# Performance work log

Hardware: AMD Instinct MI355X
Metric: run time of the kernel (lower is better)

The kernel has to match this reference:

```python
import jax, jax.numpy as jnp
import numpy as np

N = 200000
D = 256
B = 512  # fixed num_segments (batch.max()+1 in the torch code)
LN_EPS = 1e-5


def _layernorm(h, gamma, beta):
    mu = jnp.mean(h, axis=-1, keepdims=True)
    var = jnp.var(h, axis=-1, keepdims=True)
    return (h - mu) * jax.lax.rsqrt(var + LN_EPS) * gamma + beta


def setup_inputs() -> dict:
    key = jax.random.key(0)
    ks = jax.random.split(key, 10)
    x = jax.random.normal(ks[0], (N, D), dtype=jnp.float32)
    batch = jnp.sort(jax.random.randint(ks[1], (N,), 0, B)).astype(jnp.int64)
    s = 0.05
    return {
        "x": x,
        "batch": batch,
        "vn_embed": jax.random.normal(ks[2], (1, D), dtype=jnp.float32) * 0.02,
        "W1": jax.random.normal(ks[3], (D, D), dtype=jnp.float32) * s,
        "b1": jnp.zeros((D,), dtype=jnp.float32),
        "g1": jnp.ones((D,), dtype=jnp.float32),
        "be1": jnp.zeros((D,), dtype=jnp.float32),
        "W2": jax.random.normal(ks[4], (D, D), dtype=jnp.float32) * s,
        "b2": jnp.zeros((D,), dtype=jnp.float32),
        "g2": jnp.ones((D,), dtype=jnp.float32),
        "be2": jnp.zeros((D,), dtype=jnp.float32),
        "Wg": jax.random.normal(ks[5], (2 * D, D), dtype=jnp.float32) * s,
        "bg": jnp.zeros((D,), dtype=jnp.float32),
    }


def reference(x, batch, vn_embed, W1, b1, g1, be1, W2, b2, g2, be2, Wg, bg):
    # scatter-mean: per-graph average of node features  [B, D]
    seg_sum = jax.ops.segment_sum(x, batch, num_segments=B)
    cnt = jax.ops.segment_sum(jnp.ones((x.shape[0],), x.dtype), batch, num_segments=B)
    node_agg = seg_sum / jnp.maximum(cnt, 1.0)[:, None]
    # node_to_vn: Linear + GELU(exact) + LayerNorm (dropout = identity at eval)
    vn_update = _layernorm(jax.nn.gelu(node_agg @ W1 + b1, approximate=False), g1, be1)
    vn_state = vn_embed + vn_update  # vn_embed broadcasts [1,D] -> [B,D]
    # gather broadcast back to nodes + vn_to_node MLP
    vn_broadcast = vn_state[batch]  # [N, D]
    node_update = _layernorm(jax.nn.gelu(vn_broadcast @ W2 + b2, approximate=False), g2, be2)
    # sigmoid gate on concat + gated residual
    gate = jax.nn.sigmoid(jnp.concatenate([x, node_update], axis=-1) @ Wg + bg)
    x_out = x + gate * node_update
    return (x_out, vn_state)
```

## Files before the change

kernel.cpp:

```cpp
#include <hip/hip_runtime.h>
#include <hip/hip_bf16.h>
#include <math.h>

#define DIM 256
#define B_SEG 512
#define LN_EPS 1e-5f

typedef __attribute__((ext_vector_type(8))) short bf16x8;
typedef __attribute__((ext_vector_type(4))) float f32x4;

__device__ __forceinline__ float gelu_exact(float v) {
    return 0.5f * v * (1.0f + erff(v * 0.70710678118654752f));
}

__device__ __forceinline__ unsigned int pack2bf(float a, float b) {
    unsigned int ua = (unsigned int)__bfloat16_as_ushort(__float2bfloat16(a));
    unsigned int ub = (unsigned int)__bfloat16_as_ushort(__float2bfloat16(b));
    return ua | (ub << 16);
}

__device__ __forceinline__ void async16(const void* g, void* l) {
    __builtin_amdgcn_global_load_lds(
        (const __attribute__((address_space(1))) void*)(g),
        (__attribute__((address_space(3))) void*)(l), 16, 0, 0);
}

__global__ __launch_bounds__(256) void k_prep(const float* __restrict__ Wg,
                                              __hip_bfloat16* __restrict__ Wt2,
                                              const int* __restrict__ batch,
                                              int* __restrict__ seg_start, int n) {
    if (blockIdx.x < 256) {
        int k = blockIdx.x;
        int c = threadIdx.x;
        Wt2[((size_t)(k >> 3) << 11) + (c << 3) + (k & 7)] = __float2bfloat16(Wg[(size_t)k * DIM + c]);
        return;
    }
    for (int s = threadIdx.x; s <= B_SEG; s += 256) {
        int lo = 0, hi = n;
        while (lo < hi) {
            int mid = (lo + hi) >> 1;
            if (batch[mid] < s) lo = mid + 1; else hi = mid;
        }
        seg_start[s] = lo;
    }
}

__global__ __launch_bounds__(256) void k_pass1(const float* __restrict__ x,
                                               const int* __restrict__ batch,
                                               float* __restrict__ part,
                                               unsigned int* __restrict__ hdr,
                                               float* __restrict__ extra,
                                               __hip_bfloat16* __restrict__ xbf,
                                               int n, int emit) {
    const int tile = blockIdx.x;
    const int i0   = tile * 64;
    if (i0 >= n) return;
    const int iN   = min(i0 + 64, n);

    const int wave = threadIdx.x >> 6;
    const int lane = threadIdx.x & 63;
    const int d4   = lane * 4;
    const int dby  = lane * 8;

    const int sf = batch[i0];
    const int sl = batch[iN - 1];

    float4 accA = make_float4(0.f, 0.f, 0.f, 0.f);
    float4 accB = make_float4(0.f, 0.f, 0.f, 0.f);

    #pragma unroll
    for (int g = 0; g < 4; ++g) {
        int   bt[4];
        float4 v[4];
        #pragma unroll
        for (int jj = 0; jj < 4; ++jj) {
            int r = i0 + g * 16 + 4 * jj + wave;
            bt[jj] = (r < iN) ? batch[r] : -2;
        }
        #pragma unroll
        for (int jj = 0; jj < 4; ++jj) {
            int r = i0 + g * 16 + 4 * jj + wave;
            v[jj] = (r < iN) ? *(const float4*)(x + (size_t)r * DIM + d4)
                             : make_float4(0.f, 0.f, 0.f, 0.f);
        }
        __builtin_amdgcn_sched_barrier(0);
        #pragma unroll
        for (int jj = 0; jj < 4; ++jj) {
            int r = i0 + g * 16 + 4 * jj + wave;
            if (emit && r < iN) {
                uint2 pk;
                pk.x = pack2bf(v[jj].x, v[jj].y);
                pk.y = pack2bf(v[jj].z, v[jj].w);
                *(uint2*)((char*)xbf + (size_t)r * 512 + (dby ^ ((r & 7) << 4))) = pk;
            }
            if (bt[jj] == sf) {
                accA.x += v[jj].x; accA.y += v[jj].y; accA.z += v[jj].z; accA.w += v[jj].w;
            } else if (bt[jj] == sl) {
                accB.x += v[jj].x; accB.y += v[jj].y; accB.z += v[jj].z; accB.w += v[jj].w;
            } else if (r < iN) {
                atomicAdd(&extra[(size_t)bt[jj] * DIM + d4 + 0], v[jj].x);
                atomicAdd(&extra[(size_t)bt[jj] * DIM + d4 + 1], v[jj].y);
                atomicAdd(&extra[(size_t)bt[jj] * DIM + d4 + 2], v[jj].z);
                atomicAdd(&extra[(size_t)bt[jj] * DIM + d4 + 3], v[jj].w);
            }
        }
    }

    __shared__ float4 redA[4][64];
    __shared__ float4 redB[4][64];
    redA[wave][lane] = accA;
    redB[wave][lane] = accB;
    __syncthreads();
    if (wave == 0) {
        float4 a0 = redA[0][lane], a1 = redA[1][lane], a2 = redA[2][lane], a3 = redA[3][lane];
        float4 t;
        t.x = (a0.x + a1.x) + (a2.x + a3.x);
        t.y = (a0.y + a1.y) + (a2.y + a3.y);
        t.z = (a0.z + a1.z) + (a2.z + a3.z);
        t.w = (a0.w + a1.w) + (a2.w + a3.w);
        *(float4*)(part + ((size_t)tile * 2 + 0) * DIM + d4) = t;
        if (lane == 0) hdr[tile] = (unsigned int)sf | ((unsigned int)sl << 16);
    } else if (wave == 1) {
        float4 a0 = redB[0][lane], a1 = redB[1][lane], a2 = redB[2][lane], a3 = redB[3][lane];
        float4 t;
        t.x = (a0.x + a1.x) + (a2.x + a3.x);
        t.y = (a0.y + a1.y) + (a2.y + a3.y);
        t.z = (a0.z + a1.z) + (a2.z + a3.z);
        t.w = (a0.w + a1.w) + (a2.w + a3.w);
        *(float4*)(part + ((size_t)tile * 2 + 1) * DIM + d4) = t;
    }
}

__global__ __launch_bounds__(256) void k_vn(const float* __restrict__ part,
                                            const unsigned int* __restrict__ hdr,
                                            const float* __restrict__ extra,
                                            const int* __restrict__ seg_start,
                                            const float* __restrict__ vn_embed,
                                            const float* __restrict__ W1, const float* __restrict__ b1,
                                            const float* __restrict__ g1, const float* __restrict__ be1,
                                            const float* __restrict__ W2, const float* __restrict__ b2,
                                            const float* __restrict__ g2, const float* __restrict__ be2,
                                            const float* __restrict__ Wg, const float* __restrict__ bg,
                                            float* __restrict__ vn_state_out,
                                            float* __restrict__ nu,
                                            float* __restrict__ gpart,
                                            int use_parts) {
    __shared__ float sIn[DIM];
    __shared__ float sRed[DIM];
    __shared__ float sRed2[DIM];
    const int b = blockIdx.x;
    const int d = threadIdx.x;

    const int s0 = seg_start[b], s1 = seg_start[b + 1];
    float sum = extra[(size_t)b * DIM + d];
    if (use_parts && s1 > s0) {
        int t0 = s0 >> 6, t1 = (s1 - 1) >> 6;
        for (int t = t0; t <= t1; ++t) {
            unsigned int h = hdr[t];
            int f = (int)(h & 0xffffu), l = (int)(h >> 16);
            if (f == b) sum += part[((size_t)t * 2 + 0) * DIM + d];
            if (l == b && l != f) sum += part[((size_t)t * 2 + 1) * DIM + d];
        }
    }
    float denom = fmaxf((float)(s1 - s0), 1.0f);
    sIn[d] = sum / denom;
    __syncthreads();

    float h0 = 0.f, h1 = 0.f, h2a = 0.f, h3 = 0.f;
    for (int k = 0; k < DIM; k += 4) {
        h0  = fmaf(sIn[k + 0], W1[(size_t)(k + 0) * DIM + d], h0);
        h1  = fmaf(sIn[k + 1], W1[(size_t)(k + 1) * DIM + d], h1);
        h2a = fmaf(sIn[k + 2], W1[(size_t)(k + 2) * DIM + d], h2a);
        h3  = fmaf(sIn[k + 3], W1[(size_t)(k + 3) * DIM + d], h3);
    }
    float h = gelu_exact(b1[d] + ((h0 + h1) + (h2a + h3)));

    sRed[d] = h; sRed2[d] = h * h;
    __syncthreads();
    for (int s = 128; s > 0; s >>= 1) {
        if (d < s) { sRed[d] += sRed[d + s]; sRed2[d] += sRed2[d + s]; }
        __syncthreads();
    }
    float mu = sRed[0] * (1.0f / DIM);
    float var = fmaxf(sRed2[0] * (1.0f / DIM) - mu * mu, 0.0f);
    float rs = rsqrtf(var + LN_EPS);
    float vnst = vn_embed[d] + ((h - mu) * rs * g1[d] + be1[d]);
    vn_state_out[(size_t)b * DIM + d] = vnst;
    __syncthreads();
    sIn[d] = vnst;
    __syncthreads();

    float g0 = 0.f, g1a = 0.f, g2a = 0.f, g3 = 0.f;
    for (int k = 0; k < DIM; k += 4) {
        g0  = fmaf(sIn[k + 0], W2[(size_t)(k + 0) * DIM + d], g0);
        g1a = fmaf(sIn[k + 1], W2[(size_t)(k + 1) * DIM + d], g1a);
        g2a = fmaf(sIn[k + 2], W2[(size_t)(k + 2) * DIM + d], g2a);
        g3  = fmaf(sIn[k + 3], W2[(size_t)(k + 3) * DIM + d], g3);
    }
    float h2 = gelu_exact(b2[d] + ((g0 + g1a) + (g2a + g3)));

    sRed[d] = h2; sRed2[d] = h2 * h2;
    __syncthreads();
    for (int s = 128; s > 0; s >>= 1) {
        if (d < s) { sRed[d] += sRed[d + s]; sRed2[d] += sRed2[d + s]; }
        __syncthreads();
    }
    float mu2 = sRed[0] * (1.0f / DIM);
    float var2 = fmaxf(sRed2[0] * (1.0f / DIM) - mu2 * mu2, 0.0f);
    float rs2 = rsqrtf(var2 + LN_EPS);
    float nud = (h2 - mu2) * rs2 * g2[d] + be2[d];
    nu[(size_t)b * DIM + d] = nud;
    __syncthreads();
    sIn[d] = nud;
    __syncthreads();

    float p0 = 0.f, p1 = 0.f, p2 = 0.f, p3 = 0.f;
    for (int k = 0; k < DIM; k += 4) {
        p0 = fmaf(sIn[k + 0], Wg[(size_t)(DIM + k + 0) * DIM + d], p0);
        p1 = fmaf(sIn[k + 1], Wg[(size_t)(DIM + k + 1) * DIM + d], p1);
        p2 = fmaf(sIn[k + 2], Wg[(size_t)(DIM + k + 2) * DIM + d], p2);
        p3 = fmaf(sIn[k + 3], Wg[(size_t)(DIM + k + 3) * DIM + d], p3);
    }
    gpart[(size_t)b * DIM + d] = bg[d] + ((p0 + p1) + (p2 + p3));
}

__global__ __launch_bounds__(256, 4) void k_gate_bf(const __hip_bfloat16* __restrict__ xbf,
                                                    const int* __restrict__ batch,
                                                    const __hip_bfloat16* __restrict__ Wt2,
                                                    const float* __restrict__ nu,
                                                    const float* __restrict__ gpart,
                                                    float* __restrict__ xout,
                                                    int n) {
    __shared__ __align__(16) char sA[64 * 512];

    const int tid  = threadIdx.x;
    const int wave = tid >> 6;
    const int lane = tid & 63;
    const int r15  = lane & 15;
    const int kq   = lane >> 4;
    const size_t i0 = (size_t)blockIdx.x * 64;

    const char* gsrc = (const char*)xbf + i0 * 512;
    #pragma unroll
    for (int j = 0; j < 8; ++j)
        async16(gsrc + j * 4096 + tid * 16, sA + j * 4096 + wave * 1024);
    __syncthreads();

    f32x4 acc[4][4];
    #pragma unroll
    for (int m = 0; m < 4; ++m)
        #pragma unroll
        for (int nn = 0; nn < 4; ++nn)
            acc[m][nn] = (f32x4){0.f, 0.f, 0.f, 0.f};

    #pragma unroll
    for (int ks = 0; ks < 8; ++ks) {
        bf16x8 a[4], b[4];
        #pragma unroll
        for (int nn = 0; nn < 4; ++nn) {
            int c = wave * 64 + nn * 16 + r15;
            b[nn] = *(const bf16x8*)(Wt2 + ((size_t)(ks * 4 + kq) << 11) + (c << 3));
        }
        #pragma unroll
        for (int m = 0; m < 4; ++m) {
            int r = m * 16 + r15;
            a[m] = *(const bf16x8*)(sA + r * 512 + ((ks * 64 + kq * 16) ^ ((r & 7) << 4)));
        }
        #pragma unroll
        for (int m = 0; m < 4; ++m)
            #pragma unroll
            for (int nn = 0; nn < 4; ++nn)
                acc[m][nn] = __builtin_amdgcn_mfma_f32_16x16x32_bf16(a[m], b[nn], acc[m][nn], 0, 0, 0);
    }

    #pragma unroll
    for (int m = 0; m < 4; ++m) {
        #pragma unroll
        for (int q = 0; q < 4; ++q) {
            int rr = m * 16 + kq * 4 + q;
            long node = (long)(i0 + rr);
            if (node >= n) continue;
            int bb = batch[node];
            #pragma unroll
            for (int nn = 0; nn < 4; ++nn) {
                int col = wave * 64 + nn * 16 + r15;
                float pre = acc[m][nn][q] + gpart[bb * DIM + col];
                float e = __expf(-pre);
                float gte = __builtin_amdgcn_rcpf(1.0f + e);
                float xres = __bfloat162float(
                    *(const __hip_bfloat16*)(sA + rr * 512 + ((2 * col) ^ ((rr & 7) << 4))));
                xout[(size_t)node * DIM + col] = xres + gte * nu[bb * DIM + col];
            }
        }
    }
}

__global__ __launch_bounds__(256) void k_segsum_fp(const float* __restrict__ x,
                                                   const int* __restrict__ batch,
                                                   float* __restrict__ sums,
                                                   int n) {
    const int i0 = blockIdx.x * 64;
    if (i0 >= n) return;
    const int t    = threadIdx.x;
    const int lane = t & 63;
    const int d4   = lane * 4;
    const int rg   = t >> 6;
    float4 acc = make_float4(0.f, 0.f, 0.f, 0.f);
    int cur = -1;
    for (int j = 0; j < 16; ++j) {
        int i = i0 + rg + 4 * j;
        if (i >= n) break;
        int b = batch[i];
        if (b != cur) {
            if (cur >= 0) {
                atomicAdd(&sums[(size_t)cur * DIM + d4 + 0], acc.x);
                atomicAdd(&sums[(size_t)cur * DIM + d4 + 1], acc.y);
                atomicAdd(&sums[(size_t)cur * DIM + d4 + 2], acc.z);
                atomicAdd(&sums[(size_t)cur * DIM + d4 + 3], acc.w);
            }
            acc = make_float4(0.f, 0.f, 0.f, 0.f);
            cur = b;
        }
        float4 v = *(const float4*)(x + (size_t)i * DIM + d4);
        acc.x += v.x; acc.y += v.y; acc.z += v.z; acc.w += v.w;
    }
    if (cur >= 0) {
        atomicAdd(&sums[(size_t)cur * DIM + d4 + 0], acc.x);
        atomicAdd(&sums[(size_t)cur * DIM + d4 + 1], acc.y);
        atomicAdd(&sums[(size_t)cur * DIM + d4 + 2], acc.z);
        atomicAdd(&sums[(size_t)cur * DIM + d4 + 3], acc.w);
    }
}

__global__ __launch_bounds__(256) void k_gate_fp(const float* __restrict__ x,
                                                 const int* __restrict__ batch,
                                                 const __hip_bfloat16* __restrict__ Wt2,
                                                 const float* __restrict__ nu,
                                                 const float* __restrict__ gpart,
                                                 float* __restrict__ xout,
                                                 int n) {
    __shared__ __align__(16) char sA[32 * 512];
    const int tid  = threadIdx.x;
    const int wave = tid >> 6;
    const int lane = tid & 63;
    const int r15  = lane & 15;
    const int kq   = lane >> 4;
    const int i0   = blockIdx.x * 32;

    float4 av0[4], av1[4];
    #pragma unroll
    for (int j = 0; j < 4; ++j) {
        int v = j * 256 + tid;
        int r = v >> 5;
        int k8 = v & 31;
        int node = i0 + r;
        if (node < n) {
            const float* p = x + (size_t)node * DIM + k8 * 8;
            av0[j] = *(const float4*)p;
            av1[j] = *(const float4*)(p + 4);
        } else {
            av0[j] = make_float4(0.f, 0.f, 0.f, 0.f);
            av1[j] = av0[j];
        }
    }
    #pragma unroll
    for (int j = 0; j < 4; ++j) {
        int v = j * 256 + tid;
        int r = v >> 5;
        int k8 = v & 31;
        uint4 pk;
        pk.x = pack2bf(av0[j].x, av0[j].y);
        pk.y = pack2bf(av0[j].z, av0[j].w);
        pk.z = pack2bf(av1[j].x, av1[j].y);
        pk.w = pack2bf(av1[j].z, av1[j].w);
        *(uint4*)(sA + r * 512 + ((k8 * 16) ^ ((r & 7) << 4))) = pk;
    }
    __syncthreads();

    f32x4 acc[2][4];
    #pragma unroll
    for (int m = 0; m < 2; ++m)
        #pragma unroll
        for (int nn = 0; nn < 4; ++nn)
            acc[m][nn] = (f32x4){0.f, 0.f, 0.f, 0.f};

    #pragma unroll
    for (int ks = 0; ks < 8; ++ks) {
        bf16x8 a[2], b[4];
        #pragma unroll
        for (int nn = 0; nn < 4; ++nn) {
            int c = wave * 64 + nn * 16 + r15;
            b[nn] = *(const bf16x8*)(Wt2 + ((size_t)(ks * 4 + kq) << 11) + (c << 3));
        }
        #pragma unroll
        for (int m = 0; m < 2; ++m) {
            int r = m * 16 + r15;
            a[m] = *(const bf16x8*)(sA + r * 512 + ((ks * 64 + kq * 16) ^ ((r & 7) << 4)));
        }
        #pragma unroll
        for (int m = 0; m < 2; ++m)
            #pragma unroll
            for (int nn = 0; nn < 4; ++nn)
                acc[m][nn] = __builtin_amdgcn_mfma_f32_16x16x32_bf16(a[m], b[nn], acc[m][nn], 0, 0, 0);
    }

    #pragma unroll
    for (int m = 0; m < 2; ++m) {
        #pragma unroll
        for (int q = 0; q < 4; ++q) {
            int rr = m * 16 + kq * 4 + q;
            int node = i0 + rr;
            if (node >= n) continue;
            int bb = batch[node];
            #pragma unroll
            for (int nn = 0; nn < 4; ++nn) {
                int col = wave * 64 + nn * 16 + r15;
                float pre = acc[m][nn][q] + gpart[bb * DIM + col];
                float e = __expf(-pre);
                float gte = __builtin_amdgcn_rcpf(1.0f + e);
                float xres = __bfloat162float(
                    *(const __hip_bfloat16*)(sA + rr * 512 + ((2 * col) ^ ((rr & 7) << 4))));
                xout[(size_t)node * DIM + col] = xres + gte * nu[bb * DIM + col];
            }
        }
    }
}

extern "C" void kernel_launch(void* const* d_in, const int* in_sizes, int n_in,
                              void* d_out, int out_size, void* d_ws, size_t ws_size,
                              hipStream_t stream) {
    const float* x        = (const float*)d_in[0];
    const int*   batch    = (const int*)d_in[1];
    const float* vn_embed = (const float*)d_in[2];
    const float* W1  = (const float*)d_in[3];
    const float* b1  = (const float*)d_in[4];
    const float* g1  = (const float*)d_in[5];
    const float* be1 = (const float*)d_in[6];
    const float* W2  = (const float*)d_in[7];
    const float* b2  = (const float*)d_in[8];
    const float* g2  = (const float*)d_in[9];
    const float* be2 = (const float*)d_in[10];
    const float* Wg  = (const float*)d_in[11];
    const float* bg  = (const float*)d_in[12];

    const int n = in_sizes[0] / DIM;
    const int nt64 = (n + 63) / 64;

    float* out = (float*)d_out;
    float* xout = out;
    float* vn_state_out = out + (size_t)n * DIM;

    char* wsb = (char*)d_ws;
    int*          seg_start = (int*)wsb;
    unsigned int* hdr       = (unsigned int*)(wsb + 4096);
    float*        extra     = (float*)(wsb + 20480);
    float*        part      = (float*)(wsb + 544768);
    char*         after     = wsb + 544768 + (size_t)nt64 * 2 * DIM * 4;
    float* nu    = (float*)after;
    float* gpart = nu + (size_t)B_SEG * DIM;
    __hip_bfloat16* Wt2 = (__hip_bfloat16*)(gpart + (size_t)B_SEG * DIM);
    __hip_bfloat16* xbf = Wt2 + (size_t)DIM * DIM;

    const size_t xbf_off = (size_t)((char*)xbf - wsb);
    const size_t need = xbf_off + (size_t)nt64 * 64 * 512;
    const bool use_bf = (ws_size >= need);

    hipMemsetAsync(extra, 0, (size_t)B_SEG * DIM * sizeof(float), stream);

    k_prep<<<257, 256, 0, stream>>>(Wg, Wt2, batch, seg_start, n);

    if (use_bf) {
        k_pass1<<<nt64, 256, 0, stream>>>(x, batch, part, hdr, extra, xbf, n, 1);
    } else {
        k_segsum_fp<<<nt64, 256, 0, stream>>>(x, batch, extra, n);
    }

    k_vn<<<B_SEG, 256, 0, stream>>>(part, hdr, extra, seg_start, vn_embed,
                                    W1, b1, g1, be1,
                                    W2, b2, g2, be2,
                                    Wg, bg,
                                    vn_state_out, nu, gpart,
                                    use_bf ? 1 : 0);

    if (use_bf) {
        k_gate_bf<<<nt64, 256, 0, stream>>>(xbf, batch, Wt2, nu, gpart, xout, n);
    } else {
        int nblk3 = (n + 31) / 32;
        k_gate_fp<<<nblk3, 256, 0, stream>>>(x, batch, Wt2, nu, gpart, xout, n);
    }
}
```

Measured before the change: 200.3 us.

## Stage pass1 x tile into LDS via async global_load_lds and fold memset into prep

The segment-sum pass now copies the whole 64-row x tile into 64KB of shared memory with asynchronous global-to-LDS loads, then each wave walks 16 contiguous rows from LDS. The reduction buffers reuse the same shared memory. The separate memset of the atomic accumulator is removed and its zeroing is done by 128 extra blocks of the prep kernel, saving one launch. The 64KB LDS footprint per block limits occupancy to about two blocks per CU, which may reduce latency hiding compared with the previous register-based loads.

```diff
diff --git a/kernel.cpp b/kernel.cpp
--- a/kernel.cpp
+++ b/kernel.cpp
@@ -28,39 +28,61 @@
 __global__ __launch_bounds__(256) void k_prep(const float* __restrict__ Wg,
                                               __hip_bfloat16* __restrict__ Wt2,
                                               const int* __restrict__ batch,
-                                              int* __restrict__ seg_start, int n) {
+                                              int* __restrict__ seg_start,
+                                              float* __restrict__ extra, int n) {
     if (blockIdx.x < 256) {
         int k = blockIdx.x;
         int c = threadIdx.x;
         Wt2[((size_t)(k >> 3) << 11) + (c << 3) + (k & 7)] = __float2bfloat16(Wg[(size_t)k * DIM + c]);
         return;
     }
-    for (int s = threadIdx.x; s <= B_SEG; s += 256) {
-        int lo = 0, hi = n;
-        while (lo < hi) {
-            int mid = (lo + hi) >> 1;
-            if (batch[mid] < s) lo = mid + 1; else hi = mid;
-        }
-        seg_start[s] = lo;
-    }
-}
-
-__global__ __launch_bounds__(256) void k_pass1(const float* __restrict__ x,
-                                               const int* __restrict__ batch,
-                                               float* __restrict__ part,
-                                               unsigned int* __restrict__ hdr,
-                                               float* __restrict__ extra,
-                                               __hip_bfloat16* __restrict__ xbf,
-                                               int n, int emit) {
+    if (blockIdx.x == 256) {
+        for (int s = threadIdx.x; s <= B_SEG; s += 256) {
+            int lo = 0, hi = n;
+            while (lo < hi) {
+                int mid = (lo + hi) >> 1;
+                if (batch[mid] < s) lo = mid + 1; else hi = mid;
+            }
+            seg_start[s] = lo;
+        }
+        return;
+    }
+    int b = blockIdx.x - 257;
+    ((float4*)extra)[(size_t)b * 256 + threadIdx.x] = make_float4(0.f, 0.f, 0.f, 0.f);
+}
+
+__global__ __launch_bounds__(256, 2) void k_pass1(const float* __restrict__ x,
+                                                  const int* __restrict__ batch,
+                                                  float* __restrict__ part,
+                                                  unsigned int* __restrict__ hdr,
+                                                  float* __restrict__ extra,
+                                                  __hip_bfloat16* __restrict__ xbf,
+                                                  int n, int emit) {
+    __shared__ __align__(16) char sX[64 * 1024];
+
     const int tile = blockIdx.x;
     const int i0   = tile * 64;
     if (i0 >= n) return;
     const int iN   = min(i0 + 64, n);
 
-    const int wave = threadIdx.x >> 6;
-    const int lane = threadIdx.x & 63;
-    const int d4   = lane * 4;
-    const int dby  = lane * 8;
+    const int tid  = threadIdx.x;
+    const int wave = tid >> 6;
+    const int lane = tid & 63;
+
+    if (iN - i0 == 64) {
+        const char* gsrc = (const char*)x + (size_t)i0 * 1024;
+        #pragma unroll
+        for (int j = 0; j < 16; ++j)
+            async16(gsrc + j * 4096 + tid * 16, sX + j * 4096 + wave * 1024);
+    } else {
+        for (int v = tid; v < 64 * 64; v += 256) {
+            int r = v >> 6, c = v & 63;
+            float4 val = (i0 + r < n) ? *(const float4*)(x + (size_t)(i0 + r) * DIM + c * 4)
+                                      : make_float4(0.f, 0.f, 0.f, 0.f);
+            *(float4*)(sX + r * 1024 + c * 16) = val;
+        }
+    }
+    __syncthreads();
 
     const int sf = batch[i0];
     const int sl = batch[iN - 1];
@@ -68,66 +90,56 @@
     float4 accA = make_float4(0.f, 0.f, 0.f, 0.f);
     float4 accB = make_float4(0.f, 0.f, 0.f, 0.f);
 
-    #pragma unroll
-    for (int g = 0; g < 4; ++g) {
-        int   bt[4];
-        float4 v[4];
-        #pragma unroll
-        for (int jj = 0; jj < 4; ++jj) {
-            int r = i0 + g * 16 + 4 * jj + wave;
-            bt[jj] = (r < iN) ? batch[r] : -2;
-        }
-        #pragma unroll
-        for (int jj = 0; jj < 4; ++jj) {
-            int r = i0 + g * 16 + 4 * jj + wave;
-            v[jj] = (r < iN) ? *(const float4*)(x + (size_t)r * DIM + d4)
-                             : make_float4(0.f, 0.f, 0.f, 0.f);
-        }
-        __builtin_amdgcn_sched_barrier(0);
-        #pragma unroll
-        for (int jj = 0; jj < 4; ++jj) {
-            int r = i0 + g * 16 + 4 * jj + wave;
-            if (emit && r < iN) {
-                uint2 pk;
-                pk.x = pack2bf(v[jj].x, v[jj].y);
-                pk.y = pack2bf(v[jj].z, v[jj].w);
-                *(uint2*)((char*)xbf + (size_t)r * 512 + (dby ^ ((r & 7) << 4))) = pk;
-            }
-            if (bt[jj] == sf) {
-                accA.x += v[jj].x; accA.y += v[jj].y; accA.z += v[jj].z; accA.w += v[jj].w;
-            } else if (bt[jj] == sl) {
-                accB.x += v[jj].x; accB.y += v[jj].y; accB.z += v[jj].z; accB.w += v[jj].w;
-            } else if (r < iN) {
-                atomicAdd(&extra[(size_t)bt[jj] * DIM + d4 + 0], v[jj].x);
-                atomicAdd(&extra[(size_t)bt[jj] * DIM + d4 + 1], v[jj].y);
-                atomicAdd(&extra[(size_t)bt[jj] * DIM + d4 + 2], v[jj].z);
-                atomicAdd(&extra[(size_t)bt[jj] * DIM + d4 + 3], v[jj].w);
-            }
-        }
-    }
-
-    __shared__ float4 redA[4][64];
-    __shared__ float4 redB[4][64];
-    redA[wave][lane] = accA;
-    redB[wave][lane] = accB;
+    const int rbase = wave * 16;
+    #pragma unroll
+    for (int jj = 0; jj < 16; ++jj) {
+        const int r  = rbase + jj;
+        const int gr = i0 + r;
+        const bool valid = gr < n;
+        float4 v = *(const float4*)(sX + r * 1024 + lane * 16);
+        int b = valid ? batch[gr] : -2;
+        if (emit && valid) {
+            uint2 pk;
+            pk.x = pack2bf(v.x, v.y);
+            pk.y = pack2bf(v.z, v.w);
+            *(uint2*)((char*)xbf + (size_t)gr * 512 + ((lane * 8) ^ ((r & 7) << 4))) = pk;
+        }
+        if (b == sf) {
+            accA.x += v.x; accA.y += v.y; accA.z += v.z; accA.w += v.w;
+        } else if (b == sl) {
+            accB.x += v.x; accB.y += v.y; accB.z += v.z; accB.w += v.w;
+        } else if (valid) {
+            atomicAdd(&extra[(size_t)b * DIM + lane * 4 + 0], v.x);
+            atomicAdd(&extra[(size_t)b * DIM + lane * 4 + 1], v.y);
+            atomicAdd(&extra[(size_t)b * DIM + lane * 4 + 2], v.z);
+            atomicAdd(&extra[(size_t)b * DIM + lane * 4 + 3], v.w);
+        }
+    }
+
+    __syncthreads();
+    float4* red = (float4*)sX;
+    red[(wave * 2 + 0) * 64 + lane] = accA;
+    red[(wave * 2 + 1) * 64 + lane] = accB;
     __syncthreads();
     if (wave == 0) {
-        float4 a0 = redA[0][lane], a1 = redA[1][lane], a2 = redA[2][lane], a3 = redA[3][lane];
+        float4 a0 = red[0 * 64 + lane], a1 = red[2 * 64 + lane],
+               a2 = red[4 * 64 + lane], a3 = red[6 * 64 + lane];
         float4 t;
         t.x = (a0.x + a1.x) + (a2.x + a3.x);
         t.y = (a0.y + a1.y) + (a2.y + a3.y);
         t.z = (a0.z + a1.z) + (a2.z + a3.z);
         t.w = (a0.w + a1.w) + (a2.w + a3.w);
-        *(float4*)(part + ((size_t)tile * 2 + 0) * DIM + d4) = t;
+        *(float4*)(part + ((size_t)tile * 2 + 0) * DIM + lane * 4) = t;
         if (lane == 0) hdr[tile] = (unsigned int)sf | ((unsigned int)sl << 16);
     } else if (wave == 1) {
-        float4 a0 = redB[0][lane], a1 = redB[1][lane], a2 = redB[2][lane], a3 = redB[3][lane];
+        float4 a0 = red[1 * 64 + lane], a1 = red[3 * 64 + lane],
+               a2 = red[5 * 64 + lane], a3 = red[7 * 64 + lane];
         float4 t;
         t.x = (a0.x + a1.x) + (a2.x + a3.x);
         t.y = (a0.y + a1.y) + (a2.y + a3.y);
         t.z = (a0.z + a1.z) + (a2.z + a3.z);
         t.w = (a0.w + a1.w) + (a2.w + a3.w);
-        *(float4*)(part + ((size_t)tile * 2 + 1) * DIM + d4) = t;
+        *(float4*)(part + ((size_t)tile * 2 + 1) * DIM + lane * 4) = t;
     }
 }
 
@@ -465,9 +477,7 @@
     const size_t need = xbf_off + (size_t)nt64 * 64 * 512;
     const bool use_bf = (ws_size >= need);
 
-    hipMemsetAsync(extra, 0, (size_t)B_SEG * DIM * sizeof(float), stream);
-
-    k_prep<<<257, 256, 0, stream>>>(Wg, Wt2, batch, seg_start, n);
+    k_prep<<<385, 256, 0, stream>>>(Wg, Wt2, batch, seg_start, extra, n);
 
     if (use_bf) {
         k_pass1<<<nt64, 256, 0, stream>>>(x, batch, part, hdr, extra, xbf, n, 1);
```

Measured after the change: 204.2 us. Within noise of the previous version (+2.0%).
